# Performance work log

Measured on AMD Instinct MI355X. Metric: run time of the kernel, lower is better.

The kernel has to match this reference:

```python
import jax, jax.numpy as jnp
import numpy as np

NUM_HEADS = 4
HEAD_DIM = 64
BN_EPS = 1e-5


def setup_inputs() -> dict:
    key = jax.random.key(0)
    ks = jax.random.split(key, 6)
    B, C, H, W = 8, 256, 48, 48
    HD = NUM_HEADS * HEAD_DIM  # 256
    x = jax.random.normal(ks[0], (B, C, H, W), dtype=jnp.float32)
    q_w = jax.random.normal(ks[1], (HD, C), dtype=jnp.float32) * (1.0 / np.sqrt(C))
    k_w = jax.random.normal(ks[2], (HEAD_DIM, C), dtype=jnp.float32) * (1.0 / np.sqrt(C))
    v_w = jax.random.normal(ks[3], (HEAD_DIM, C), dtype=jnp.float32) * (1.0 / np.sqrt(C))
    proj_w = jax.random.normal(ks[4], (C, HD), dtype=jnp.float32) * (1.0 / np.sqrt(HD))
    proj_b = jnp.zeros((C,), dtype=jnp.float32)
    gamma = jnp.ones((C,), dtype=jnp.float32)
    beta = jnp.zeros((C,), dtype=jnp.float32)
    return {"x": x, "q_w": q_w, "k_w": k_w, "v_w": v_w,
            "proj_w": proj_w, "proj_b": proj_b, "gamma": gamma, "beta": beta}


def reference(x, q_w, k_w, v_w, proj_w, proj_b, gamma, beta):
    B, C, H, W = x.shape
    N = H * W
    scale = HEAD_DIM ** -0.5
    xf = x.reshape(B, C, N)  # 1x1 conv == channel matmul
    q = jnp.einsum('oc,bcn->bon', q_w, xf).reshape(B, NUM_HEADS, HEAD_DIM, N)
    k = jnp.einsum('dc,bcn->bdn', k_w, xf)  # shared single KV head (MQA)
    v = jnp.einsum('dc,bcn->bdn', v_w, xf)
    # scores: [B, heads, N, N]
    attn = jnp.einsum('bhdn,bdm->bhnm', q, k) * scale
    attn = jax.nn.softmax(attn, axis=-1)
    out = jnp.einsum('bhnm,bdm->bhdn', attn, v)  # [B, heads, d, N]
    out = out.reshape(B, NUM_HEADS * HEAD_DIM, N)
    out = jnp.einsum('co,bon->bcn', proj_w, out) + proj_b[None, :, None]
    out = out.reshape(B, C, H, W)
    # BatchNorm2d (training-mode batch statistics, biased variance)
    mean = jnp.mean(out, axis=(0, 2, 3), keepdims=True)
    var = jnp.var(out, axis=(0, 2, 3), keepdims=True)
    out = gamma[None, :, None, None] * (out - mean) * jax.lax.rsqrt(var + BN_EPS) + beta[None, :, None, None]
    return out + x
```

## Files before the change

kernel.cpp:

```cpp
#include <hip/hip_runtime.h>
#include <hip/hip_bf16.h>
#include <math.h>

#define BB 8
#define CCH 256
#define NN 2304
#define NH 4
#define HDIM 64
#define QKV_ROWS 384
#define BN_EPS 1e-5f
#define NTILES 36
#define HTILES 18
#define NPART 576
#define SLOG2E 0.18033688011112042f

typedef short bf16x8 __attribute__((ext_vector_type(8)));
typedef short bf16x4 __attribute__((ext_vector_type(4)));
typedef float f32x4 __attribute__((ext_vector_type(4)));

#if __has_builtin(__builtin_amdgcn_exp2f)
#define EXP2(x) __builtin_amdgcn_exp2f(x)
#else
#define EXP2(x) __expf((x) * 0.6931471805599453f)
#endif

#define MFMA16(a, b, c) __builtin_amdgcn_mfma_f32_16x16x16bf16_1k(a, b, c, 0, 0, 0)
#define MFMA32(a, b, c) __builtin_amdgcn_mfma_f32_16x16x32_bf16(a, b, c, 0, 0, 0)

__device__ __forceinline__ unsigned bfpair(float a, float b) {
    __hip_bfloat162 h = __float22bfloat162_rn(make_float2(a, b));
    return *(unsigned*)&h;
}
__device__ __forceinline__ unsigned short f2bf(float f) {
    unsigned u = __float_as_uint(f);
    u = (u + 0x7FFFu + ((u >> 16) & 1u)) >> 16;
    return (unsigned short)u;
}
__device__ __forceinline__ bf16x4 pack4(float p0, float p1, float p2, float p3) {
    union { unsigned u[2]; bf16x4 v; } x;
    x.u[0] = bfpair(p0, p1);
    x.u[1] = bfpair(p2, p3);
    return x.v;
}
__device__ __forceinline__ float bf2f(unsigned short s) {
    return __uint_as_float((unsigned)s << 16);
}

__global__ __launch_bounds__(256) void prep_k(
    const float* __restrict__ x,
    const float* __restrict__ qw, const float* __restrict__ kw,
    const float* __restrict__ vw, const float* __restrict__ pw,
    unsigned short* __restrict__ xT,
    unsigned short* __restrict__ Wb, unsigned short* __restrict__ Pb)
{
    const int bid = blockIdx.x;
    const int tid = threadIdx.x;
    if (bid < 1152) {
        __shared__ float sX[64][65];
        const int b  = bid / 144;
        const int rem = bid - b * 144;
        const int nb = (rem >> 2) * 64;
        const int cb = (rem & 3) * 64;

        #pragma unroll
        for (int u = 0; u < 4; ++u) {
            int c  = (tid >> 4) + 16 * u;
            int n4 = (tid & 15) * 4;
            float4 v = *(const float4*)(x + ((size_t)(b * CCH + cb + c)) * NN + nb + n4);
            sX[c][n4+0] = v.x; sX[c][n4+1] = v.y; sX[c][n4+2] = v.z; sX[c][n4+3] = v.w;
        }
        __syncthreads();

        const int n  = tid >> 2;
        const int cg = (tid & 3) * 16;
        unsigned vals[8];
        #pragma unroll
        for (int p = 0; p < 8; ++p)
            vals[p] = bfpair(sX[cg + 2*p][n], sX[cg + 2*p + 1][n]);
        unsigned short* dst = xT + ((size_t)(b * NN + nb + n)) * CCH + cb + cg;
        *(uint4*)dst = make_uint4(vals[0], vals[1], vals[2], vals[3]);
        *(uint4*)(dst + 8) = make_uint4(vals[4], vals[5], vals[6], vals[7]);
    } else {
        int idx = (bid - 1152) * 256 + tid;
        if (idx < 98304) {
            int o = idx >> 8, c = idx & 255;
            float v;
            if (o < 256)      v = qw[(size_t)o * CCH + c] * SLOG2E;
            else if (o < 320) v = kw[(size_t)(o - 256) * CCH + c];
            else              v = vw[(size_t)(o - 320) * CCH + c];
            Wb[idx] = f2bf(v);
        } else {
            int j = idx - 98304;
            if (j < 65536) Pb[j] = f2bf(pw[j]);
        }
    }
}

__global__ __launch_bounds__(128) void qkv_mfma_k(
    const unsigned short* __restrict__ Wb, const unsigned short* __restrict__ xT,
    unsigned short* __restrict__ Qt, unsigned short* __restrict__ Kt,
    unsigned short* __restrict__ Vn)
{
    __shared__ unsigned short sE[2][64 * 40];
    const int tid = threadIdx.x;
    const int wave = tid >> 6;
    const int lane = tid & 63;
    const int quad = lane >> 4;
    const int l15  = lane & 15;
    const int b  = blockIdx.x;
    const int nb = blockIdx.y * 32;
    const int mb = blockIdx.z * 128 + wave * 64;

    const unsigned short* Ab = Wb + (size_t)(mb + l15) * CCH + quad * 8;
    const unsigned short* Bb = xT + ((size_t)(b * NN + nb + l15)) * CCH + quad * 8;

    f32x4 C[4][2] = {};
    bf16x8 aA[2][4], bB[2][2];
    #pragma unroll
    for (int i = 0; i < 4; ++i) aA[0][i] = *(const bf16x8*)(Ab + (size_t)(16*i) * CCH);
    #pragma unroll
    for (int j = 0; j < 2; ++j) bB[0][j] = *(const bf16x8*)(Bb + (size_t)(16*j) * CCH);

    #pragma unroll
    for (int kk = 0; kk < 8; ++kk) {
        const int cur = kk & 1;
        if (kk < 7) {
            const int k1 = (kk + 1) * 32;
            #pragma unroll
            for (int i = 0; i < 4; ++i) aA[cur^1][i] = *(const bf16x8*)(Ab + (size_t)(16*i) * CCH + k1);
            #pragma unroll
            for (int j = 0; j < 2; ++j) bB[cur^1][j] = *(const bf16x8*)(Bb + (size_t)(16*j) * CCH + k1);
        }
        #pragma unroll
        for (int i = 0; i < 4; ++i)
            #pragma unroll
            for (int j = 0; j < 2; ++j)
                C[i][j] = MFMA32(aA[cur][i], bB[cur][j], C[i][j]);
    }

    unsigned short* sEw = &sE[wave][0];
    if (mb < 320) {
        #pragma unroll
        for (int i = 0; i < 4; ++i)
            #pragma unroll
            for (int j = 0; j < 2; ++j) {
                unsigned p01 = bfpair(C[i][j][0], C[i][j][1]);
                unsigned p23 = bfpair(C[i][j][2], C[i][j][3]);
                unsigned short* p = sEw + (16*j + l15) * 72 + 16*i + quad*4;
                *(unsigned*)p = p01;
                *(unsigned*)(p + 2) = p23;
            }
        if (mb < 256) {
            #pragma unroll
            for (int it = 0; it < 4; ++it) {
                int flat = lane + 64 * it;
                int row = flat >> 3;
                int o8  = (flat & 7) * 8;
                uint4 v = *(const uint4*)(sEw + row * 72 + o8);
                *(uint4*)(Qt + ((size_t)(b * NN + nb + row)) * CCH + mb + o8) = v;
            }
        } else {
            #pragma unroll
            for (int it = 0; it < 4; ++it) {
                int flat = lane + 64 * it;
                int row = flat >> 3;
                int o8  = (flat & 7) * 8;
                uint4 v = *(const uint4*)(sEw + row * 72 + o8);
                *(uint4*)(Kt + ((size_t)(b * NN + nb + row)) * 64 + o8) = v;
            }
        }
    } else {
        #pragma unroll
        for (int i = 0; i < 4; ++i)
            #pragma unroll
            for (int j = 0; j < 2; ++j) {
                unsigned p01 = bfpair(C[i][j][0], C[i][j][1]);
                unsigned p23 = bfpair(C[i][j][2], C[i][j][3]);
                unsigned short* p = sEw + (16*i + quad*4) * 40 + 16*j + l15;
                p[0]   = (unsigned short)p01;
                p[40]  = (unsigned short)(p01 >> 16);
                p[80]  = (unsigned short)p23;
                p[120] = (unsigned short)(p23 >> 16);
            }
        #pragma unroll
        for (int it = 0; it < 4; ++it) {
            int flat = lane + 64 * it;
            int row = flat >> 2;
            int n8  = (flat & 3) * 8;
            uint4 v = *(const uint4*)(sEw + row * 40 + n8);
            *(uint4*)(Vn + ((size_t)(b * 64 + (mb - 320) + row)) * NN + nb + n8) = v;
        }
    }
}

__global__ __launch_bounds__(512, 4) void attn_k(
    const unsigned short* __restrict__ Qt,
    const unsigned short* __restrict__ Kt,
    const unsigned short* __restrict__ Vn,
    unsigned short* __restrict__ Ao)
{
    __shared__ __align__(16) unsigned short sKV[4 * 64 * 72];

    const int tid   = threadIdx.x;
    const int wave  = tid >> 6;
    const int lane  = tid & 63;
    const int quad  = lane >> 4;
    const int l15   = lane & 15;
    const int qslot = wave & 1;
    const int kh    = (wave >> 1) & 1;
    const int hloc  = wave >> 2;
    const int qoff  = qslot * 32;
    const int b     = blockIdx.x;
    const int nb    = blockIdx.y * 64;
    const int head  = blockIdx.z * 2 + hloc;

    unsigned short* sKb = sKV + kh * 2 * 4608;
    unsigned short* sVb = sKb + 4608;

    const bf16x4 vone = {(short)0x3F80, (short)0x3F80, (short)0x3F80, (short)0x3F80};

    bf16x8 bQ[2][2];
    const unsigned short* QtB = Qt + ((size_t)(b * NN + nb + qoff + l15)) * CCH + head * 64 + quad * 8;
    #pragma unroll
    for (int qt = 0; qt < 2; ++qt)
        #pragma unroll
        for (int s = 0; s < 2; ++s)
            bQ[qt][s] = *(const bf16x8*)(QtB + (size_t)(16*qt) * CCH + s * 32);

    const int srow = tid >> 3;
    const int sch8 = (tid & 7) * 8;
    bf16x8 pf[4];
    #pragma unroll
    for (int u = 0; u < 4; ++u) {
        const int keys0 = (u >> 1) * HTILES * 64;
        if ((u & 1) == 0)
            pf[u] = *(const bf16x8*)(Kt + ((size_t)(b * NN + keys0 + srow)) * 64 + sch8);
        else
            pf[u] = *(const bf16x8*)(Vn + ((size_t)(b * 64 + srow)) * NN + keys0 + sch8);
    }

    f32x4 O[4][2] = {};
    f32x4 dacc[2] = {};

    for (int step = 0; step < HTILES; ++step) {
        __syncthreads();
        #pragma unroll
        for (int u = 0; u < 4; ++u)
            *(bf16x8*)(sKV + u * 4608 + srow * 72 + sch8) = pf[u];
        __syncthreads();

        if (step + 1 < HTILES) {
            #pragma unroll
            for (int u = 0; u < 4; ++u) {
                const int keys0 = ((u >> 1) * HTILES + step + 1) * 64;
                if ((u & 1) == 0)
                    pf[u] = *(const bf16x8*)(Kt + ((size_t)(b * NN + keys0 + srow)) * 64 + sch8);
                else
                    pf[u] = *(const bf16x8*)(Vn + ((size_t)(b * 64 + srow)) * NN + keys0 + sch8);
            }
        }

        f32x4 C[4][2] = {};
        #pragma unroll
        for (int s = 0; s < 2; ++s)
            #pragma unroll
            for (int kt = 0; kt < 4; ++kt) {
                bf16x8 aK = *(const bf16x8*)(sKb + (16*kt + l15) * 72 + s * 32 + quad * 8);
                C[kt][0] = MFMA32(aK, bQ[0][s], C[kt][0]);
                C[kt][1] = MFMA32(aK, bQ[1][s], C[kt][1]);
            }

        bf16x4 bP[4][2];
        #pragma unroll
        for (int kt = 0; kt < 4; ++kt)
            #pragma unroll
            for (int qt = 0; qt < 2; ++qt)
                bP[kt][qt] = pack4(EXP2(C[kt][qt][0]), EXP2(C[kt][qt][1]),
                                   EXP2(C[kt][qt][2]), EXP2(C[kt][qt][3]));

        #pragma unroll
        for (int kt = 0; kt < 4; ++kt) {
            dacc[0] = MFMA16(vone, bP[kt][0], dacc[0]);
            dacc[1] = MFMA16(vone, bP[kt][1], dacc[1]);
        }

        #pragma unroll
        for (int jd = 0; jd < 4; ++jd)
            #pragma unroll
            for (int kt = 0; kt < 4; ++kt) {
                bf16x4 aV = *(const bf16x4*)(sVb + (16*jd + l15) * 72 + 16*kt + quad*4);
                O[jd][0] = MFMA16(aV, bP[kt][0], O[jd][0]);
                O[jd][1] = MFMA16(aV, bP[kt][1], O[jd][1]);
            }
    }
    __syncthreads();

    float* sc = (float*)sKV;
    const int base = (hloc * 2 + qslot) * 2304 + lane * 36;
    if (kh == 1) {
        #pragma unroll
        for (int jd = 0; jd < 4; ++jd)
            #pragma unroll
            for (int qt = 0; qt < 2; ++qt)
                *(f32x4*)(sc + base + jd * 8 + qt * 4) = O[jd][qt];
        sc[base + 32] = dacc[0][0];
        sc[base + 33] = dacc[1][0];
    }
    __syncthreads();
    float rinv[2] = {0.f, 0.f};
    if (kh == 0) {
        #pragma unroll
        for (int jd = 0; jd < 4; ++jd)
            #pragma unroll
            for (int qt = 0; qt < 2; ++qt)
                O[jd][qt] += *(const f32x4*)(sc + base + jd * 8 + qt * 4);
        rinv[0] = 1.0f / (dacc[0][0] + sc[base + 32]);
        rinv[1] = 1.0f / (dacc[1][0] + sc[base + 33]);
    }
    __syncthreads();

    unsigned short* sT = (unsigned short*)sKV;
    if (kh == 0) {
        #pragma unroll
        for (int qt = 0; qt < 2; ++qt)
            #pragma unroll
            for (int jd = 0; jd < 4; ++jd) {
                unsigned lo = bfpair(O[jd][qt][0] * rinv[qt], O[jd][qt][1] * rinv[qt]);
                unsigned hi = bfpair(O[jd][qt][2] * rinv[qt], O[jd][qt][3] * rinv[qt]);
                *(uint2*)(sT + (hloc * 64 + qoff + 16*qt + l15) * 72 + 16*jd + quad*4) = make_uint2(lo, hi);
            }
    }
    __syncthreads();

    #pragma unroll
    for (int it = 0; it < 2; ++it) {
        int flat = tid + 512 * it;
        int hh   = flat >> 9;
        int row  = (flat >> 3) & 63;
        int c8   = (flat & 7) * 8;
        uint4 v = *(const uint4*)(sT + (hh * 64 + row) * 72 + c8);
        *(uint4*)(Ao + ((size_t)(b * NN + nb + row)) * CCH + (blockIdx.z * 2 + hh) * 64 + c8) = v;
    }
}

__global__ __launch_bounds__(128) void proj_mfma_k(
    const unsigned short* __restrict__ Pb, const unsigned short* __restrict__ Ao,
    const float* __restrict__ pb, unsigned short* __restrict__ projb,
    float* __restrict__ psum, float* __restrict__ psq)
{
    __shared__ unsigned short sE[2][64 * 40];
    const int tid = threadIdx.x;
    const int wave = tid >> 6;
    const int lane = tid & 63;
    const int quad = lane >> 4;
    const int l15  = lane & 15;
    const int b  = blockIdx.x;
    const int nb = blockIdx.y * 32;
    const int mb = blockIdx.z * 128 + wave * 64;
    const int part = b * 72 + blockIdx.y;

    const unsigned short* Ab = Pb + (size_t)(mb + l15) * CCH + quad * 8;
    const unsigned short* Bb = Ao + ((size_t)(b * NN + nb + l15)) * CCH + quad * 8;

    f32x4 C[4][2] = {};
    bf16x8 aA[2][4], bB[2][2];
    #pragma unroll
    for (int i = 0; i < 4; ++i) aA[0][i] = *(const bf16x8*)(Ab + (size_t)(16*i) * CCH);
    #pragma unroll
    for (int j = 0; j < 2; ++j) bB[0][j] = *(const bf16x8*)(Bb + (size_t)(16*j) * CCH);

    #pragma unroll
    for (int kk = 0; kk < 8; ++kk) {
        const int cur = kk & 1;
        if (kk < 7) {
            const int k1 = (kk + 1) * 32;
            #pragma unroll
            for (int i = 0; i < 4; ++i) aA[cur^1][i] = *(const bf16x8*)(Ab + (size_t)(16*i) * CCH + k1);
            #pragma unroll
            for (int j = 0; j < 2; ++j) bB[cur^1][j] = *(const bf16x8*)(Bb + (size_t)(16*j) * CCH + k1);
        }
        #pragma unroll
        for (int i = 0; i < 4; ++i)
            #pragma unroll
            for (int j = 0; j < 2; ++j)
                C[i][j] = MFMA32(aA[cur][i], bB[cur][j], C[i][j]);
    }

    unsigned short* sEw = &sE[wave][0];
    #pragma unroll
    for (int i = 0; i < 4; ++i) {
        #pragma unroll
        for (int r = 0; r < 4; ++r) {
            const int ch = mb + 16*i + quad*4 + r;
            const float bias = pb[ch];
            float v0 = C[i][0][r] + bias, v1 = C[i][1][r] + bias;
            C[i][0][r] = v0; C[i][1][r] = v1;
            float rs = v0 + v1;
            float rq = v0*v0 + v1*v1;
            rs += __shfl_xor(rs, 1); rq += __shfl_xor(rq, 1);
            rs += __shfl_xor(rs, 2); rq += __shfl_xor(rq, 2);
            rs += __shfl_xor(rs, 4); rq += __shfl_xor(rq, 4);
            rs += __shfl_xor(rs, 8); rq += __shfl_xor(rq, 8);
            if (l15 == 0) {
                psum[(size_t)ch * NPART + part] = rs;
                psq [(size_t)ch * NPART + part] = rq;
            }
        }
    }

    #pragma unroll
    for (int i = 0; i < 4; ++i)
        #pragma unroll
        for (int j = 0; j < 2; ++j) {
            unsigned p01 = bfpair(C[i][j][0], C[i][j][1]);
            unsigned p23 = bfpair(C[i][j][2], C[i][j][3]);
            unsigned short* p = sEw + (16*i + quad*4) * 40 + 16*j + l15;
            p[0]   = (unsigned short)p01;
            p[40]  = (unsigned short)(p01 >> 16);
            p[80]  = (unsigned short)p23;
            p[120] = (unsigned short)(p23 >> 16);
        }
    #pragma unroll
    for (int it = 0; it < 4; ++it) {
        int flat = lane + 64 * it;
        int row = flat >> 2;
        int n8  = (flat & 3) * 8;
        uint4 v = *(const uint4*)(sEw + row * 40 + n8);
        *(uint4*)(projb + ((size_t)(b * CCH + mb + row)) * NN + nb + n8) = v;
    }
}

__global__ __launch_bounds__(64) void bn_finalize_k(
    const float* __restrict__ psum, const float* __restrict__ psq,
    const float* __restrict__ gamma, const float* __restrict__ beta,
    float* __restrict__ stats)
{
    const int c = blockIdx.x;
    const int lane = threadIdx.x;
    float s = 0.f, q = 0.f;
    for (int k = lane; k < NPART; k += 64) {
        s += psum[(size_t)c * NPART + k];
        q += psq [(size_t)c * NPART + k];
    }
    #pragma unroll
    for (int off = 1; off < 64; off <<= 1) {
        s += __shfl_xor(s, off);
        q += __shfl_xor(q, off);
    }
    if (lane == 0) {
        const float inv_n = 1.0f / (float)(BB * NN);
        float mean = s * inv_n;
        float var  = q * inv_n - mean * mean;
        float sc = gamma[c] * rsqrtf(var + BN_EPS);
        stats[c] = sc;
        stats[CCH + c] = beta[c] - mean * sc;
    }
}

__global__ __launch_bounds__(256) void bn_apply_k(
    const unsigned short* __restrict__ projb, const float* __restrict__ x,
    const float* __restrict__ stats, float* __restrict__ out)
{
    size_t idx = ((size_t)blockIdx.x * 256 + threadIdx.x) * 8;
    const size_t total = (size_t)BB * CCH * NN;
    if (idx >= total) return;
    int c = (int)((idx / NN) % CCH);
    float sc = stats[c], sh = stats[CCH + c];
    uint4 pv = *(const uint4*)(projb + idx);
    const unsigned short* ps = (const unsigned short*)&pv;
    float4 x0 = *(const float4*)(x + idx);
    float4 x1 = *(const float4*)(x + idx + 4);
    float4 r0, r1;
    r0.x = sc * bf2f(ps[0]) + sh + x0.x;
    r0.y = sc * bf2f(ps[1]) + sh + x0.y;
    r0.z = sc * bf2f(ps[2]) + sh + x0.z;
    r0.w = sc * bf2f(ps[3]) + sh + x0.w;
    r1.x = sc * bf2f(ps[4]) + sh + x1.x;
    r1.y = sc * bf2f(ps[5]) + sh + x1.y;
    r1.z = sc * bf2f(ps[6]) + sh + x1.z;
    r1.w = sc * bf2f(ps[7]) + sh + x1.w;
    *(float4*)(out + idx) = r0;
    *(float4*)(out + idx + 4) = r1;
}

extern "C" void kernel_launch(void* const* d_in, const int* in_sizes, int n_in,
                              void* d_out, int out_size, void* d_ws, size_t ws_size,
                              hipStream_t stream)
{
    const float* x     = (const float*)d_in[0];
    const float* qw    = (const float*)d_in[1];
    const float* kw    = (const float*)d_in[2];
    const float* vw    = (const float*)d_in[3];
    const float* pw    = (const float*)d_in[4];
    const float* pb    = (const float*)d_in[5];
    const float* gamma = (const float*)d_in[6];
    const float* beta  = (const float*)d_in[7];
    float* out = (float*)d_out;

    char* ws = (char*)d_ws;
    unsigned short* xT = (unsigned short*)ws;
    unsigned short* Ao = (unsigned short*)ws;
    unsigned short* Wb = (unsigned short*)(ws + 9437184);
    unsigned short* Pb = (unsigned short*)(ws + 9633792);
    unsigned short* Qt = (unsigned short*)(ws + 9764864);
    unsigned short* Kt = (unsigned short*)(ws + 19202048);
    unsigned short* Vn = (unsigned short*)(ws + 21561344);
    unsigned short* projb = (unsigned short*)(ws + 9764864);
    float* stats = (float*)(ws + 28639232);
    float* psum  = (float*)(ws + 28641280);
    float* psq   = (float*)(ws + 29231104);

    prep_k<<<1792, 256, 0, stream>>>(x, qw, kw, vw, pw, xT, Wb, Pb);

    dim3 g1(BB, 72, 3);
    qkv_mfma_k<<<g1, 128, 0, stream>>>(Wb, xT, Qt, Kt, Vn);

    dim3 g2(BB, NN / 64, NH / 2);
    attn_k<<<g2, 512, 0, stream>>>(Qt, Kt, Vn, Ao);

    dim3 g3(BB, 72, 2);
    proj_mfma_k<<<g3, 128, 0, stream>>>(Pb, Ao, pb, projb, psum, psq);

    bn_finalize_k<<<CCH, 64, 0, stream>>>(psum, psq, gamma, beta, stats);

    int total8 = BB * CCH * NN / 8;
    bn_apply_k<<<(total8 + 255) / 256, 256, 0, stream>>>(projb, x, stats, out);
}
```

Before: 208.9 us.

## Widen GEMM N-tiles, fuse BN finalize into apply, read bf16 residual

Doubles the N tile of the QKV and projection MFMA kernels from 32 to 64 columns, halving the number of BN partial sums. Removes the separate BN finalize kernel by having each (batch, channel) block of the apply kernel reduce the partial statistics itself. prep_k additionally writes a bf16 copy of x, which the apply kernel reads as the residual instead of fp32 x. This trades an extra write in prep and redundant stat reductions for fewer launches and smaller residual reads, with some added precision loss in the residual.

Result: faster. 200.8 us (-3.9%).

```diff
diff --git a/kernel.cpp b/kernel.cpp
--- a/kernel.cpp
+++ b/kernel.cpp
@@ -11,7 +11,7 @@
 #define BN_EPS 1e-5f
 #define NTILES 36
 #define HTILES 18
-#define NPART 576
+#define NPART 288
 #define SLOG2E 0.18033688011112042f
 
 typedef short bf16x8 __attribute__((ext_vector_type(8)));
@@ -50,7 +50,7 @@
     const float* __restrict__ x,
     const float* __restrict__ qw, const float* __restrict__ kw,
     const float* __restrict__ vw, const float* __restrict__ pw,
-    unsigned short* __restrict__ xT,
+    unsigned short* __restrict__ xT, unsigned short* __restrict__ xb,
     unsigned short* __restrict__ Wb, unsigned short* __restrict__ Pb)
 {
     const int bid = blockIdx.x;
@@ -80,6 +80,19 @@
         unsigned short* dst = xT + ((size_t)(b * NN + nb + n)) * CCH + cb + cg;
         *(uint4*)dst = make_uint4(vals[0], vals[1], vals[2], vals[3]);
         *(uint4*)(dst + 8) = make_uint4(vals[4], vals[5], vals[6], vals[7]);
+
+        #pragma unroll
+        for (int it = 0; it < 2; ++it) {
+            int flat = tid + 256 * it;
+            int row = flat >> 3;
+            int n8  = (flat & 7) * 8;
+            unsigned vv[4];
+            #pragma unroll
+            for (int p = 0; p < 4; ++p)
+                vv[p] = bfpair(sX[row][n8 + 2*p], sX[row][n8 + 2*p + 1]);
+            *(uint4*)(xb + ((size_t)(b * CCH + cb + row)) * NN + nb + n8) =
+                make_uint4(vv[0], vv[1], vv[2], vv[3]);
+        }
     } else {
         int idx = (bid - 1152) * 256 + tid;
         if (idx < 98304) {
@@ -101,25 +114,25 @@
     unsigned short* __restrict__ Qt, unsigned short* __restrict__ Kt,
     unsigned short* __restrict__ Vn)
 {
-    __shared__ unsigned short sE[2][64 * 40];
+    __shared__ unsigned short sE[2][64 * 72];
     const int tid = threadIdx.x;
     const int wave = tid >> 6;
     const int lane = tid & 63;
     const int quad = lane >> 4;
     const int l15  = lane & 15;
     const int b  = blockIdx.x;
-    const int nb = blockIdx.y * 32;
+    const int nb = blockIdx.y * 64;
     const int mb = blockIdx.z * 128 + wave * 64;
 
     const unsigned short* Ab = Wb + (size_t)(mb + l15) * CCH + quad * 8;
     const unsigned short* Bb = xT + ((size_t)(b * NN + nb + l15)) * CCH + quad * 8;
 
-    f32x4 C[4][2] = {};
-    bf16x8 aA[2][4], bB[2][2];
+    f32x4 C[4][4] = {};
+    bf16x8 aA[2][4], bB[2][4];
     #pragma unroll
     for (int i = 0; i < 4; ++i) aA[0][i] = *(const bf16x8*)(Ab + (size_t)(16*i) * CCH);
     #pragma unroll
-    for (int j = 0; j < 2; ++j) bB[0][j] = *(const bf16x8*)(Bb + (size_t)(16*j) * CCH);
+    for (int j = 0; j < 4; ++j) bB[0][j] = *(const bf16x8*)(Bb + (size_t)(16*j) * CCH);
 
     #pragma unroll
     for (int kk = 0; kk < 8; ++kk) {
@@ -129,12 +142,12 @@
             #pragma unroll
             for (int i = 0; i < 4; ++i) aA[cur^1][i] = *(const bf16x8*)(Ab + (size_t)(16*i) * CCH + k1);
             #pragma unroll
-            for (int j = 0; j < 2; ++j) bB[cur^1][j] = *(const bf16x8*)(Bb + (size_t)(16*j) * CCH + k1);
+            for (int j = 0; j < 4; ++j) bB[cur^1][j] = *(const bf16x8*)(Bb + (size_t)(16*j) * CCH + k1);
         }
         #pragma unroll
         for (int i = 0; i < 4; ++i)
             #pragma unroll
-            for (int j = 0; j < 2; ++j)
+            for (int j = 0; j < 4; ++j)
                 C[i][j] = MFMA32(aA[cur][i], bB[cur][j], C[i][j]);
     }
 
@@ -143,7 +156,7 @@
         #pragma unroll
         for (int i = 0; i < 4; ++i)
             #pragma unroll
-            for (int j = 0; j < 2; ++j) {
+            for (int j = 0; j < 4; ++j) {
                 unsigned p01 = bfpair(C[i][j][0], C[i][j][1]);
                 unsigned p23 = bfpair(C[i][j][2], C[i][j][3]);
                 unsigned short* p = sEw + (16*j + l15) * 72 + 16*i + quad*4;
@@ -152,7 +165,7 @@
             }
         if (mb < 256) {
             #pragma unroll
-            for (int it = 0; it < 4; ++it) {
+            for (int it = 0; it < 8; ++it) {
                 int flat = lane + 64 * it;
                 int row = flat >> 3;
                 int o8  = (flat & 7) * 8;
@@ -161,7 +174,7 @@
             }
         } else {
             #pragma unroll
-            for (int it = 0; it < 4; ++it) {
+            for (int it = 0; it < 8; ++it) {
                 int flat = lane + 64 * it;
                 int row = flat >> 3;
                 int o8  = (flat & 7) * 8;
@@ -173,21 +186,21 @@
         #pragma unroll
         for (int i = 0; i < 4; ++i)
             #pragma unroll
-            for (int j = 0; j < 2; ++j) {
+            for (int j = 0; j < 4; ++j) {
                 unsigned p01 = bfpair(C[i][j][0], C[i][j][1]);
                 unsigned p23 = bfpair(C[i][j][2], C[i][j][3]);
-                unsigned short* p = sEw + (16*i + quad*4) * 40 + 16*j + l15;
+                unsigned short* p = sEw + (16*i + quad*4) * 72 + 16*j + l15;
                 p[0]   = (unsigned short)p01;
-                p[40]  = (unsigned short)(p01 >> 16);
-                p[80]  = (unsigned short)p23;
-                p[120] = (unsigned short)(p23 >> 16);
-            }
-        #pragma unroll
-        for (int it = 0; it < 4; ++it) {
+                p[72]  = (unsigned short)(p01 >> 16);
+                p[144] = (unsigned short)p23;
+                p[216] = (unsigned short)(p23 >> 16);
+            }
+        #pragma unroll
+        for (int it = 0; it < 8; ++it) {
             int flat = lane + 64 * it;
-            int row = flat >> 2;
-            int n8  = (flat & 3) * 8;
-            uint4 v = *(const uint4*)(sEw + row * 40 + n8);
+            int row = flat >> 3;
+            int n8  = (flat & 7) * 8;
+            uint4 v = *(const uint4*)(sEw + row * 72 + n8);
             *(uint4*)(Vn + ((size_t)(b * 64 + (mb - 320) + row)) * NN + nb + n8) = v;
         }
     }
@@ -348,26 +361,26 @@
     const float* __restrict__ pb, unsigned short* __restrict__ projb,
     float* __restrict__ psum, float* __restrict__ psq)
 {
-    __shared__ unsigned short sE[2][64 * 40];
+    __shared__ unsigned short sE[2][64 * 72];
     const int tid = threadIdx.x;
     const int wave = tid >> 6;
     const int lane = tid & 63;
     const int quad = lane >> 4;
     const int l15  = lane & 15;
     const int b  = blockIdx.x;
-    const int nb = blockIdx.y * 32;
+    const int nb = blockIdx.y * 64;
     const int mb = blockIdx.z * 128 + wave * 64;
-    const int part = b * 72 + blockIdx.y;
+    const int part = b * NTILES + blockIdx.y;
 
     const unsigned short* Ab = Pb + (size_t)(mb + l15) * CCH + quad * 8;
     const unsigned short* Bb = Ao + ((size_t)(b * NN + nb + l15)) * CCH + quad * 8;
 
-    f32x4 C[4][2] = {};
-    bf16x8 aA[2][4], bB[2][2];
+    f32x4 C[4][4] = {};
+    bf16x8 aA[2][4], bB[2][4];
     #pragma unroll
     for (int i = 0; i < 4; ++i) aA[0][i] = *(const bf16x8*)(Ab + (size_t)(16*i) * CCH);
     #pragma unroll
-    for (int j = 0; j < 2; ++j) bB[0][j] = *(const bf16x8*)(Bb + (size_t)(16*j) * CCH);
+    for (int j = 0; j < 4; ++j) bB[0][j] = *(const bf16x8*)(Bb + (size_t)(16*j) * CCH);
 
     #pragma unroll
     for (int kk = 0; kk < 8; ++kk) {
@@ -377,12 +390,12 @@
             #pragma unroll
             for (int i = 0; i < 4; ++i) aA[cur^1][i] = *(const bf16x8*)(Ab + (size_t)(16*i) * CCH + k1);
             #pragma unroll
-            for (int j = 0; j < 2; ++j) bB[cur^1][j] = *(const bf16x8*)(Bb + (size_t)(16*j) * CCH + k1);
+            for (int j = 0; j < 4; ++j) bB[cur^1][j] = *(const bf16x8*)(Bb + (size_t)(16*j) * CCH + k1);
         }
         #pragma unroll
         for (int i = 0; i < 4; ++i)
             #pragma unroll
-            for (int j = 0; j < 2; ++j)
+            for (int j = 0; j < 4; ++j)
                 C[i][j] = MFMA32(aA[cur][i], bB[cur][j], C[i][j]);
     }
 
@@ -394,9 +407,10 @@
             const int ch = mb + 16*i + quad*4 + r;
             const float bias = pb[ch];
             float v0 = C[i][0][r] + bias, v1 = C[i][1][r] + bias;
-            C[i][0][r] = v0; C[i][1][r] = v1;
-            float rs = v0 + v1;
-            float rq = v0*v0 + v1*v1;
+            float v2 = C[i][2][r] + bias, v3 = C[i][3][r] + bias;
+            C[i][0][r] = v0; C[i][1][r] = v1; C[i][2][r] = v2; C[i][3][r] = v3;
+            float rs = (v0 + v1) + (v2 + v3);
+            float rq = (v0*v0 + v1*v1) + (v2*v2 + v3*v3);
             rs += __shfl_xor(rs, 1); rq += __shfl_xor(rq, 1);
             rs += __shfl_xor(rs, 2); rq += __shfl_xor(rq, 2);
             rs += __shfl_xor(rs, 4); rq += __shfl_xor(rq, 4);
@@ -411,76 +425,75 @@
     #pragma unroll
     for (int i = 0; i < 4; ++i)
         #pragma unroll
-        for (int j = 0; j < 2; ++j) {
+        for (int j = 0; j < 4; ++j) {
             unsigned p01 = bfpair(C[i][j][0], C[i][j][1]);
             unsigned p23 = bfpair(C[i][j][2], C[i][j][3]);
-            unsigned short* p = sEw + (16*i + quad*4) * 40 + 16*j + l15;
+            unsigned short* p = sEw + (16*i + quad*4) * 72 + 16*j + l15;
             p[0]   = (unsigned short)p01;
-            p[40]  = (unsigned short)(p01 >> 16);
-            p[80]  = (unsigned short)p23;
-            p[120] = (unsigned short)(p23 >> 16);
-        }
-    #pragma unroll
-    for (int it = 0; it < 4; ++it) {
+            p[72]  = (unsigned short)(p01 >> 16);
+            p[144] = (unsigned short)p23;
+            p[216] = (unsigned short)(p23 >> 16);
+        }
+    #pragma unroll
+    for (int it = 0; it < 8; ++it) {
         int flat = lane + 64 * it;
-        int row = flat >> 2;
-        int n8  = (flat & 3) * 8;
-        uint4 v = *(const uint4*)(sEw + row * 40 + n8);
+        int row = flat >> 3;
+        int n8  = (flat & 7) * 8;
+        uint4 v = *(const uint4*)(sEw + row * 72 + n8);
         *(uint4*)(projb + ((size_t)(b * CCH + mb + row)) * NN + nb + n8) = v;
     }
 }
 
-__global__ __launch_bounds__(64) void bn_finalize_k(
+__global__ __launch_bounds__(256) void bn_apply_k(
+    const unsigned short* __restrict__ projb, const unsigned short* __restrict__ xb,
     const float* __restrict__ psum, const float* __restrict__ psq,
     const float* __restrict__ gamma, const float* __restrict__ beta,
-    float* __restrict__ stats)
+    float* __restrict__ out)
 {
-    const int c = blockIdx.x;
-    const int lane = threadIdx.x;
+    const int tid = threadIdx.x;
+    const int b = blockIdx.x;
+    const int c = blockIdx.y;
+
     float s = 0.f, q = 0.f;
-    for (int k = lane; k < NPART; k += 64) {
+    for (int k = tid; k < NPART; k += 256) {
         s += psum[(size_t)c * NPART + k];
         q += psq [(size_t)c * NPART + k];
     }
-    #pragma unroll
-    for (int off = 1; off < 64; off <<= 1) {
-        s += __shfl_xor(s, off);
-        q += __shfl_xor(q, off);
-    }
-    if (lane == 0) {
-        const float inv_n = 1.0f / (float)(BB * NN);
-        float mean = s * inv_n;
-        float var  = q * inv_n - mean * mean;
-        float sc = gamma[c] * rsqrtf(var + BN_EPS);
-        stats[c] = sc;
-        stats[CCH + c] = beta[c] - mean * sc;
-    }
-}
-
-__global__ __launch_bounds__(256) void bn_apply_k(
-    const unsigned short* __restrict__ projb, const float* __restrict__ x,
-    const float* __restrict__ stats, float* __restrict__ out)
-{
-    size_t idx = ((size_t)blockIdx.x * 256 + threadIdx.x) * 8;
-    const size_t total = (size_t)BB * CCH * NN;
-    if (idx >= total) return;
-    int c = (int)((idx / NN) % CCH);
-    float sc = stats[c], sh = stats[CCH + c];
-    uint4 pv = *(const uint4*)(projb + idx);
-    const unsigned short* ps = (const unsigned short*)&pv;
-    float4 x0 = *(const float4*)(x + idx);
-    float4 x1 = *(const float4*)(x + idx + 4);
-    float4 r0, r1;
-    r0.x = sc * bf2f(ps[0]) + sh + x0.x;
-    r0.y = sc * bf2f(ps[1]) + sh + x0.y;
-    r0.z = sc * bf2f(ps[2]) + sh + x0.z;
-    r0.w = sc * bf2f(ps[3]) + sh + x0.w;
-    r1.x = sc * bf2f(ps[4]) + sh + x1.x;
-    r1.y = sc * bf2f(ps[5]) + sh + x1.y;
-    r1.z = sc * bf2f(ps[6]) + sh + x1.z;
-    r1.w = sc * bf2f(ps[7]) + sh + x1.w;
-    *(float4*)(out + idx) = r0;
-    *(float4*)(out + idx + 4) = r1;
+    __shared__ float rs[256], rq[256];
+    rs[tid] = s; rq[tid] = q;
+    __syncthreads();
+    for (int off = 128; off > 0; off >>= 1) {
+        if (tid < off) { rs[tid] += rs[tid + off]; rq[tid] += rq[tid + off]; }
+        __syncthreads();
+    }
+    const float inv_n = 1.0f / (float)(BB * NN);
+    float mean = rs[0] * inv_n;
+    float var  = rq[0] * inv_n - mean * mean;
+    float scv = gamma[c] * rsqrtf(var + BN_EPS);
+    float shv = beta[c] - mean * scv;
+
+    #pragma unroll
+    for (int it = 0; it < 2; ++it) {
+        int chunk = tid + 256 * it;
+        if (chunk < 288) {
+            size_t base = ((size_t)(b * CCH + c)) * NN + chunk * 8;
+            uint4 pv = *(const uint4*)(projb + base);
+            uint4 xv = *(const uint4*)(xb + base);
+            const unsigned short* pp = (const unsigned short*)&pv;
+            const unsigned short* xx = (const unsigned short*)&xv;
+            float4 r0, r1;
+            r0.x = scv * bf2f(pp[0]) + shv + bf2f(xx[0]);
+            r0.y = scv * bf2f(pp[1]) + shv + bf2f(xx[1]);
+            r0.z = scv * bf2f(pp[2]) + shv + bf2f(xx[2]);
+            r0.w = scv * bf2f(pp[3]) + shv + bf2f(xx[3]);
+            r1.x = scv * bf2f(pp[4]) + shv + bf2f(xx[4]);
+            r1.y = scv * bf2f(pp[5]) + shv + bf2f(xx[5]);
+            r1.z = scv * bf2f(pp[6]) + shv + bf2f(xx[6]);
+            r1.w = scv * bf2f(pp[7]) + shv + bf2f(xx[7]);
+            *(float4*)(out + base) = r0;
+            *(float4*)(out + base + 4) = r1;
+        }
+    }
 }
 
 extern "C" void kernel_launch(void* const* d_in, const int* in_sizes, int n_in,
@@ -506,23 +519,21 @@
     unsigned short* Kt = (unsigned short*)(ws + 19202048);
     unsigned short* Vn = (unsigned short*)(ws + 21561344);
     unsigned short* projb = (unsigned short*)(ws + 9764864);
-    float* stats = (float*)(ws + 28639232);
-    float* psum  = (float*)(ws + 28641280);
-    float* psq   = (float*)(ws + 29231104);
-
-    prep_k<<<1792, 256, 0, stream>>>(x, qw, kw, vw, pw, xT, Wb, Pb);
-
-    dim3 g1(BB, 72, 3);
+    float* psum  = (float*)(ws + 28639232);
+    float* psq   = (float*)(ws + 28934144);
+    unsigned short* xb = (unsigned short*)(ws + 29229056);
+
+    prep_k<<<1792, 256, 0, stream>>>(x, qw, kw, vw, pw, xT, xb, Wb, Pb);
+
+    dim3 g1(BB, NN / 64, 3);
     qkv_mfma_k<<<g1, 128, 0, stream>>>(Wb, xT, Qt, Kt, Vn);
 
     dim3 g2(BB, NN / 64, NH / 2);
     attn_k<<<g2, 512, 0, stream>>>(Qt, Kt, Vn, Ao);
 
-    dim3 g3(BB, 72, 2);
+    dim3 g3(BB, NN / 64, 2);
     proj_mfma_k<<<g3, 128, 0, stream>>>(Pb, Ao, pb, projb, psum, psq);
 
-    bn_finalize_k<<<CCH, 64, 0, stream>>>(psum, psq, gamma, beta, stats);
-
-    int total8 = BB * CCH * NN / 8;
-    bn_apply_k<<<(total8 + 255) / 256, 256, 0, stream>>>(projb, x, stats, out);
-}
+    dim3 g4(BB, CCH);
+    bn_apply_k<<<g4, 256, 0, stream>>>(projb, xb, psum, psq, gamma, beta, out);
+}
```
